# Optimization experiments

Measured on AMD Instinct MI355X. Metric: run time of the kernel, lower is better.

Reference implementation:

```python
import jax, jax.numpy as jnp
import numpy as np
from jax import lax

# --- static dims (match init_kwargs) ---
B = 16
Y, M, WIN = 10, 12, 48          # input_years, months_per_year, num_windows_per_month
T = Y * M * WIN                  # 5760 encoder timesteps
DENC = 256                       # encoder hidden size
U = 128                          # att_single_dense_units (bahdanau dim)
A1, A2 = 64, 32                  # att_single_dense_1st/2nd
K = 8                            # monthly/yearly num_kernels
KS, MPOOL, YPOOL = 3, 2, 2       # kernel_size, pool sizes (strides=1, VALID)
AMY = 64                         # att_mon_year_dense_1st
RNN = 256                        # RNN_num_units
FDEC = 64                        # dec_input features
NOUT = 64                        # n_output_features
# conv/pool output sizes (VALID conv, VALID pool stride 1)
H1, W1 = WIN - KS + 1 - MPOOL + 1, U - KS + 1 - MPOOL + 1      # 45, 125
H2, W2 = H1 - KS + 1 - MPOOL + 1, W1 - KS + 1 - MPOOL + 1      # 42, 122
FLATM = H2 * W2 * K                                            # 40992
HY, WY = M * H1 - KS + 1 - YPOOL + 1, W1 - KS + 1 - YPOOL + 1  # 537, 122
FLATY = HY * WY * K                                            # 524112


def conv_tanh(x, k, b):
    # Keras Conv2D(valid, activation='tanh'), NHWC/HWIO
    y = lax.conv_general_dilated(x, k, (1, 1), 'VALID',
                                 dimension_numbers=('NHWC', 'HWIO', 'NHWC'))
    return jnp.tanh(y + b)


def maxpool(x, p):
    # MaxPooling2D(pool_size=p, strides=1, valid)
    return lax.reduce_window(x, -jnp.inf, lax.max, (1, p, p, 1), (1, 1, 1, 1), 'VALID')


def setup_inputs() -> dict:
    key = jax.random.key(0)
    ks = jax.random.split(key, 24)
    r = lambda i, shape, s=0.02: jax.random.normal(ks[i], shape, jnp.float32) * s
    return {
        'dec_input': jax.random.normal(ks[0], (B, 1, FDEC), jnp.float32),
        'S_prev_dec': jax.random.normal(ks[1], (B, RNN), jnp.float32),
        'C_prev_dec': jax.random.normal(ks[2], (B, RNN), jnp.float32),
        'h_enc': jax.random.normal(ks[3], (B, T, DENC), jnp.float32),
        # attention_single params (all use_bias=False)
        'W_enc': r(4, (DENC, U)), 'W_dec': r(5, (RNN, U)),
        'W_att1': r(6, (U, A1)), 'W_att2': r(7, (A1, A2)), 'W_att3': r(8, (A2, 1)),
        # conv_pool layers
        'conv1_k': r(9, (KS, KS, 1, K)), 'conv1_b': jnp.zeros((K,), jnp.float32),
        'conv2_k': r(10, (KS, KS, K, K)), 'conv2_b': jnp.zeros((K,), jnp.float32),
        'convy_k': r(11, (KS, KS, K, K)), 'convy_b': jnp.zeros((K,), jnp.float32),
        # monthly / yearly attention denses (use_bias=True)
        'Wm1': r(12, (FLATM, AMY)), 'bm1': jnp.zeros((AMY,), jnp.float32),
        'Wm2': r(13, (AMY, 1)), 'bm2': jnp.zeros((1,), jnp.float32),
        'Wy1': r(14, (FLATY, AMY)), 'by1': jnp.zeros((AMY,), jnp.float32),
        'Wy2': r(15, (AMY, 1)), 'by2': jnp.zeros((1,), jnp.float32),
        # LSTM (input dim = DENC + FDEC); gate order i,f,g,o as in Keras
        'W_lstm': r(16, (DENC + FDEC, 4 * RNN)), 'U_lstm': r(17, (RNN, 4 * RNN)),
        'b_lstm': jnp.zeros((4 * RNN,), jnp.float32),
        # output dense
        'W_out': r(18, (RNN, NOUT)), 'b_out': jnp.zeros((NOUT,), jnp.float32),
    }


def reference(dec_input, S_prev_dec, C_prev_dec, h_enc,
              W_enc, W_dec, W_att1, W_att2, W_att3,
              conv1_k, conv1_b, conv2_k, conv2_b, convy_k, convy_b,
              Wm1, bm1, Wm2, bm2, Wy1, by1, Wy2, by2,
              W_lstm, U_lstm, b_lstm, W_out, b_out):
    # --- Bahdanau additive attention over all T encoder steps ---
    bah = h_enc @ W_enc + (S_prev_dec @ W_dec)[:, None, :]          # [B,T,U]
    e = jax.nn.relu(jax.nn.relu(jnp.tanh(bah @ W_att1) @ W_att2) @ W_att3)  # [B,T,1]
    aw = jax.nn.softmax(e, axis=1)[..., 0]                          # [B,T]
    # --- monthly conv-pool attention, batched over all Y*M month slices ---
    x = bah.reshape(B * Y * M, WIN, U, 1)
    c1 = maxpool(conv_tanh(x, conv1_k, conv1_b), MPOOL)             # [BYM,H1,W1,K]
    c2 = maxpool(conv_tanh(c1, conv2_k, conv2_b), MPOOL)            # [BYM,H2,W2,K]
    em = jax.nn.relu(jnp.tanh(c2.reshape(B * Y * M, FLATM) @ Wm1 + bm1) @ Wm2 + bm2)
    m_att = jax.nn.softmax(em.reshape(B, Y, M), axis=2)             # softmax over months
    # --- yearly conv-pool attention (months concatenated along height) ---
    yin = c1.reshape(B * Y, M * H1, W1, K)
    cy = maxpool(conv_tanh(yin, convy_k, convy_b), YPOOL)           # [BY,HY,WY,K]
    ey = jax.nn.relu(jnp.tanh(cy.reshape(B * Y, FLATY) @ Wy1 + by1) @ Wy2 + by2)
    y_att = jax.nn.softmax(ey.reshape(B, Y), axis=1)                # softmax over years
    # --- hierarchical combination of weights ---
    new_w = (aw.reshape(B, Y, M, WIN) * m_att[..., None]
             * y_att[:, :, None, None]).reshape(B, T)               # [B,T]
    ctx = jnp.einsum('bt,btd->bd', new_w, h_enc)                    # context [B,DENC]
    # --- single LSTM step on [context ; dec_input] ---
    xt = jnp.concatenate([ctx[:, None, :], dec_input], axis=-1)[:, 0, :]
    z = xt @ W_lstm + S_prev_dec @ U_lstm + b_lstm
    i, f, g, o = jnp.split(z, 4, axis=-1)
    c_new = jax.nn.sigmoid(f) * C_prev_dec + jax.nn.sigmoid(i) * jnp.tanh(g)
    h_new = jax.nn.sigmoid(o) * jnp.tanh(c_new)
    out = jax.nn.relu(h_new[:, None, :] @ W_out + b_out)            # [B,1,NOUT]
    return out, h_new, c_new, new_w
```

## Files before the change

kernel.cpp:

```cpp
#include <hip/hip_runtime.h>
#include <hip/hip_bf16.h>

#define DEV static __device__ __forceinline__

#define B_    16
#define Y_    10
#define M_    12
#define WIN_  48
#define T_    5760
#define DENC_ 256
#define U_    128
#define A1_   64
#define A2_   32
#define K_    8
#define RNN_  256
#define FDEC_ 64
#define NOUT_ 64

#define H1_   45
#define W1_   125
#define H2_   42
#define W2_   122
#define FLATM_ 40992
#define HY_   537
#define WY_   122
#define FLATY_ 524112
#define NSM_  1920
#define NSY_  160

typedef __attribute__((ext_vector_type(8))) short s16x8;
typedef __attribute__((ext_vector_type(4))) short s16x4;
typedef __attribute__((ext_vector_type(4))) float f32x4;

DEV float tanh_fast(float x){
  x = fminf(fmaxf(x, -15.0f), 15.0f);
  float e = __expf(2.0f*x);
  return (e - 1.0f) / (e + 1.0f);
}
DEV float tanh_nc(float x){
  float e = __expf(2.0f*x);
  return 1.0f - 2.0f/(e + 1.0f);
}
DEV float sigm(float x){ return 1.0f / (1.0f + __expf(-x)); }
DEV float wredsum(float v){
  #pragma unroll
  for (int off=32; off; off>>=1) v += __shfl_xor(v, off, 64);
  return v;
}
DEV short f2b(float f){
  __hip_bfloat16 h = __float2bfloat16(f);
  return *reinterpret_cast<short*>(&h);
}
DEV float b2f(short s){
  unsigned int x = ((unsigned int)(unsigned short)s) << 16;
  return __uint_as_float(x);
}
DEV unsigned int cvt_pk_bf16(float lo, float hi){
  unsigned int r;
  asm("v_cvt_pk_bf16_f32 %0, %1, %2" : "=v"(r) : "v"(lo), "v"(hi));
  return r;
}
DEV unsigned int swz_xor1u(unsigned int v){
  return (unsigned int)__builtin_amdgcn_ds_swizzle((int)v, 0x041F);
}
DEV unsigned int permb(unsigned int hi_src, unsigned int lo_src, unsigned int sel){
  return __builtin_amdgcn_perm(hi_src, lo_src, sel);
}

__global__ void k_cvt_bf16(const float* __restrict__ src, short* __restrict__ dst, long n4){
  long i = (long)blockIdx.x*256 + threadIdx.x;
  if (i < n4){
    f32x4 v = *(const f32x4*)(src + i*4);
    s16x4 o;
    #pragma unroll
    for (int q=0;q<4;q++) o[q] = f2b(v[q]);
    *(s16x4*)(dst + i*4) = o;
  }
}

__global__ void k_sdec(const float* __restrict__ S, const float* __restrict__ Wd,
                       float* __restrict__ sdec){
  int b = blockIdx.x, u = threadIdx.x;
  const float* s = S + b*DENC_;
  float acc = 0.f;
  #pragma unroll 4
  for (int d=0; d<DENC_; d++) acc += s[d]*Wd[d*U_+u];
  sdec[b*U_+u] = acc;
}

__global__ __launch_bounds__(256)
void k_bah_mfma(const float* __restrict__ h_enc, const short* __restrict__ Wenc_bf,
                const float* __restrict__ sdec, short* __restrict__ bah16){
  __shared__ short Wl[128*136];
  int tid = threadIdx.x;
  int m0 = blockIdx.x * 64;
  int lane = tid & 63, wid = tid >> 6;
  int pl = lane & 15, g = lane >> 4;
  long arow = m0 + wid*16 + pl;
  const float* ap = h_enc + arow*DENC_;
  f32x4 acc[8];
  #pragma unroll
  for (int i=0;i<8;i++) acc[i] = (f32x4){0.f,0.f,0.f,0.f};

  for (int kh=0; kh<2; kh++){
    for (int i=tid; i<16384; i+=256){
      int k = i >> 7, c = i & 127;
      Wl[c*136 + k] = Wenc_bf[(kh*128 + k)*U_ + c];
    }
    __syncthreads();
    #pragma unroll
    for (int kk=0; kk<4; kk++){
      f32x4 a0 = *(const f32x4*)(ap + kh*128 + kk*32 + g*8);
      f32x4 a1 = *(const f32x4*)(ap + kh*128 + kk*32 + g*8 + 4);
      s16x8 a;
      #pragma unroll
      for (int q=0;q<4;q++){ a[q] = f2b(a0[q]); a[4+q] = f2b(a1[q]); }
      #pragma unroll
      for (int nt=0; nt<8; nt++){
        s16x8 b = *(const s16x8*)(Wl + (nt*16+pl)*136 + kk*32 + g*8);
        acc[nt] = __builtin_amdgcn_mfma_f32_16x16x32_bf16(a, b, acc[nt], 0,0,0);
      }
    }
    __syncthreads();
  }
  int b = m0 / T_;
  #pragma unroll
  for (int nt=0; nt<8; nt++){
    float sd = sdec[b*U_ + nt*16 + pl];
    #pragma unroll
    for (int q=0; q<4; q++){
      long r = m0 + wid*16 + g*4 + q;
      bah16[r*U_ + nt*16 + pl] = f2b(acc[nt][q] + sd);
    }
  }
}

__global__ __launch_bounds__(256)
void k_att_mfma(const short* __restrict__ bah16, const float* __restrict__ W1,
                const float* __restrict__ W2, const float* __restrict__ W3f,
                float* __restrict__ e_out){
  __shared__ short W1l[64*136];
  __shared__ short W2l[32*72];
  __shared__ float hl[64][68];
  __shared__ float w3s[32];
  int tid = threadIdx.x;
  int lane = tid & 63, wid = tid >> 6;
  int pl = lane & 15, g = lane >> 4;
  long m0 = (long)blockIdx.x * 64;

  for (int i=tid; i<8192; i+=256){ int k=i>>6, c=i&63; W1l[c*136+k] = f2b(W1[k*64+c]); }
  for (int i=tid; i<2048; i+=256){ int k=i>>5, c=i&31; W2l[c*72+k]  = f2b(W2[k*32+c]); }
  if (tid < 32) w3s[tid] = W3f[tid];
  __syncthreads();

  const short* Ab = bah16 + (m0 + wid*16 + pl)*U_;
  f32x4 acc1[4];
  #pragma unroll
  for (int i=0;i<4;i++) acc1[i]=(f32x4){0.f,0.f,0.f,0.f};
  #pragma unroll
  for (int kk=0; kk<4; kk++){
    s16x8 a = *(const s16x8*)(Ab + kk*32 + g*8);
    #pragma unroll
    for (int nt=0; nt<4; nt++){
      s16x8 b = *(const s16x8*)(&W1l[(nt*16+pl)*136 + kk*32 + g*8]);
      acc1[nt] = __builtin_amdgcn_mfma_f32_16x16x32_bf16(a, b, acc1[nt], 0,0,0);
    }
  }
  #pragma unroll
  for (int nt=0; nt<4; nt++)
    #pragma unroll
    for (int q=0; q<4; q++)
      hl[wid*16 + g*4 + q][nt*16 + pl] = tanh_fast(acc1[nt][q]);
  __syncthreads();

  f32x4 acc2[2];
  #pragma unroll
  for (int i=0;i<2;i++) acc2[i]=(f32x4){0.f,0.f,0.f,0.f};
  #pragma unroll
  for (int kk=0; kk<2; kk++){
    f32x4 h0 = *(const f32x4*)(&hl[wid*16+pl][kk*32 + g*8]);
    f32x4 h1 = *(const f32x4*)(&hl[wid*16+pl][kk*32 + g*8 + 4]);
    s16x8 a;
    #pragma unroll
    for (int q=0;q<4;q++){ a[q]=f2b(h0[q]); a[4+q]=f2b(h1[q]); }
    #pragma unroll
    for (int nt=0; nt<2; nt++){
      s16x8 b = *(const s16x8*)(&W2l[(nt*16+pl)*72 + kk*32 + g*8]);
      acc2[nt] = __builtin_amdgcn_mfma_f32_16x16x32_bf16(a, b, acc2[nt], 0,0,0);
    }
  }
  #pragma unroll
  for (int q=0; q<4; q++){
    float v = fmaxf(acc2[0][q],0.f)*w3s[pl] + fmaxf(acc2[1][q],0.f)*w3s[16+pl];
    #pragma unroll
    for (int off=1; off<16; off<<=1) v += __shfl_xor(v, off, 64);
    if (pl == 0) e_out[m0 + wid*16 + g*4 + q] = fmaxf(v, 0.f);
  }
}

__global__ __launch_bounds__(256)
void k_softmax(const float* __restrict__ e, float* __restrict__ aw){
  int b = blockIdx.x, tid = threadIdx.x;
  __shared__ float red[4];
  const float* eb = e + (long)b*T_;
  float m = -1e30f;
  for (int t=tid; t<T_; t+=256) m = fmaxf(m, eb[t]);
  #pragma unroll
  for (int off=32; off; off>>=1) m = fmaxf(m, __shfl_xor(m, off, 64));
  if ((tid&63)==0) red[tid>>6] = m;
  __syncthreads();
  m = fmaxf(fmaxf(red[0],red[1]), fmaxf(red[2],red[3]));
  __syncthreads();
  float s = 0.f;
  for (int t=tid; t<T_; t+=256) s += __expf(eb[t]-m);
  s = wredsum(s);
  if ((tid&63)==0) red[tid>>6] = s;
  __syncthreads();
  s = red[0]+red[1]+red[2]+red[3];
  float inv = 1.0f/s;
  float* awb = aw + (long)b*T_;
  for (int t=tid; t<T_; t+=256) awb[t] = __expf(eb[t]-m)*inv;
}

__global__ __launch_bounds__(256)
void k_conv1s(const short* __restrict__ bah16, const float* __restrict__ k1,
              const float* __restrict__ b1, short* __restrict__ c1){
  int n = blockIdx.x >> 1, s = blockIdx.x & 1;
  int rp0 = s ? 23 : 0;
  int rp1 = s ? 44 : 22;
  int nin = rp1 + 4 - rp0;
  int tid = threadIdx.x;
  int lane = tid & 63, wid = tid >> 6;
  int c  = lane & 7;
  int wb = wid*8 + (lane >> 3);
  __shared__ float x[26][132];
  const short* xb = bah16 + (long)n*48*128 + rp0*128;
  for (int i=tid; i<nin*128; i+=256) x[i>>7][i&127] = b2f(xb[i]);
  for (int i=tid; i<26*4; i+=256)   x[i>>2][128+(i&3)] = 0.f;
  __syncthreads();

  float wk[9];
  #pragma unroll
  for (int p=0; p<9; p++) wk[p] = k1[p*8 + c];
  float bo = b1[c];
  bool odd = (c & 1);
  int qa = odd ? 2 : 0;
  bool va = (4*wb + qa)     <= 124;
  bool vb = (4*wb + qa + 1) <= 124;

  float rA[7], rB[7], rC[7];
  auto ldrow = [&](int rr, float* d){
    f32x4 a  = *(const f32x4*)(&x[rr][4*wb]);
    f32x4 b4 = *(const f32x4*)(&x[rr][4*wb+4]);
    d[0]=a[0]; d[1]=a[1]; d[2]=a[2]; d[3]=a[3]; d[4]=b4[0]; d[5]=b4[1]; d[6]=b4[2];
  };
  ldrow(0, rA); ldrow(1, rB);
  short* ob = c1 + (long)n*45*1000 + (long)rp0*1000;
  float vpc[4] = {0.f,0.f,0.f,0.f};
  int ncr = rp1 - rp0 + 2;

  for (int rr=0; rr<ncr; ++rr){
    ldrow(rr+2, rC);
    float cv[5];
    #pragma unroll
    for (int q=0; q<5; q++){
      cv[q] = bo + rA[q]*wk[0] + rA[q+1]*wk[1] + rA[q+2]*wk[2]
                 + rB[q]*wk[3] + rB[q+1]*wk[4] + rB[q+2]*wk[5]
                 + rC[q]*wk[6] + rC[q+1]*wk[7] + rC[q+2]*wk[8];
    }
    float wcv[4];
    #pragma unroll
    for (int q=0; q<4; q++) wcv[q] = fmaxf(cv[q], cv[q+1]);
    if (rr > 0){
      float t0 = tanh_nc(fmaxf(vpc[0], wcv[0]));
      float t1 = tanh_nc(fmaxf(vpc[1], wcv[1]));
      float t2 = tanh_nc(fmaxf(vpc[2], wcv[2]));
      float t3 = tanh_nc(fmaxf(vpc[3], wcv[3]));
      unsigned int A  = cvt_pk_bf16(t0, t1);
      unsigned int Bp = cvt_pk_bf16(t2, t3);
      unsigned int An = swz_xor1u(A);
      unsigned int Bn = swz_xor1u(Bp);
      unsigned int ph = odd ? Bp : An;
      unsigned int pw = odd ? Bn : A;
      unsigned int w0 = permb(ph, pw, 0x05040100u);
      unsigned int w1 = permb(ph, pw, 0x07060302u);
      long rbase = (long)(rr-1)*1000 + (c & ~1);
      if (va) *(unsigned int*)(ob + rbase + (4*wb+qa)*8)   = w0;
      if (vb) *(unsigned int*)(ob + rbase + (4*wb+qa+1)*8) = w1;
    }
    #pragma unroll
    for (int q=0; q<4; q++) vpc[q] = wcv[q];
    #pragma unroll
    for (int q=0; q<7; q++){ rA[q]=rB[q]; rB[q]=rC[q]; }
  }
}

#define LOADF(SL, OFF) { fa[SL] = *(const s16x8*)(gp + (OFF)); \
                         fb[SL] = *(const s16x8*)(gp + (OFF) + 128); }
#define CONVROW(SA,SB,SC, A0, A1) {                                          \
    A0 = (f32x4){0.f,0.f,0.f,0.f}; A1 = A0;                                  \
    A0 = __builtin_amdgcn_mfma_f32_16x16x32_bf16(fa[SA], bw[0], A0,0,0,0);   \
    A0 = __builtin_amdgcn_mfma_f32_16x16x32_bf16(fa[SB], bw[1], A0,0,0,0);   \
    A0 = __builtin_amdgcn_mfma_f32_16x16x32_bf16(fa[SC], bw[2], A0,0,0,0);   \
    A1 = __builtin_amdgcn_mfma_f32_16x16x32_bf16(fb[SA], bw[0], A1,0,0,0);   \
    A1 = __builtin_amdgcn_mfma_f32_16x16x32_bf16(fb[SB], bw[1], A1,0,0,0);   \
    A1 = __builtin_amdgcn_mfma_f32_16x16x32_bf16(fb[SC], bw[2], A1,0,0,0); }
#define PHASE(P) {                                                           \
    int ldr_ = base + (P) + 3; if (ldr_ > pmax_in) ldr_ = pmax_in;           \
    LOADF(((P)+3)&3, (long)(ldr_ - base)*1000);                              \
    f32x4 a0_, a1_;                                                          \
    CONVROW((P)&3, ((P)+1)&3, ((P)+2)&3, a0_, a1_);                          \
    epi(a0_, a1_, opg + (P)*976, base + (P));                                \
  }

__global__ __launch_bounds__(256)
void k_convf(const short* __restrict__ c1,
             const float* __restrict__ k2, const float* __restrict__ b2,
             const float* __restrict__ ky, const float* __restrict__ by,
             short* __restrict__ c2m, short* __restrict__ cy){
  int s  = blockIdx.x & 1;
  int nm = blockIdx.x >> 1;
  int n = nm / 12, m = nm % 12;
  int tid = threadIdx.x, lane = tid & 63, wid = tid >> 6;
  int pl = lane & 15, g = lane >> 4;
  bool isY = (pl >= 8);
  int ch = pl & 7;
  bool odd = (ch & 1);

  int rl_end = (m < 11) ? 45 : 42;
  int ps0 = s ? 23 : 0;
  int p1  = s ? rl_end : 23;
  int pmax_in = p1 + 2;

  const float* kern = isY ? ky : k2;
  s16x8 bw[3];
  #pragma unroll
  for (int dy=0; dy<3; dy++){
    #pragma unroll
    for (int i=0; i<8; i++){
      int k = g*8 + i;
      bw[dy][i] = (k < 24) ? f2b(kern[(dy*24 + k)*8 + ch]) : (short)0;
    }
  }
  float bo = isY ? by[ch] : b2[ch];

  int Tw = 31*wid;
  int qa = odd ? 2 : 0;
  int s0off = (Tw + g*4 + qa)*8 + (ch & ~1);
  bool v1a = (Tw + 16 + g*4 + qa)     <= 121;
  bool v1b = ((Tw + 16 + g*4 + qa + 1) <= 121) && !(odd && g == 3);
  int bpa16 = ((lane+16)&63)*4;
  int bpaPL = pl*4;

  const short* gp = c1 + ((long)n*540 + 45*m + ps0)*1000 + (size_t)((Tw + pl + g)*8);
  short* opg = isY ? (cy  + ((long)n*537 + (long)45*m + ps0 - 1)*976)
                   : (c2m + ((long)(n*12+m)*42 + ps0 - 1)*976);

  s16x8 fa[4], fb[4];
  LOADF(0, 0);
  LOADF(1, 1000);
  LOADF(2, 2000);

  float vp[8];
  #pragma unroll
  for (int i=0;i<8;i++) vp[i]=0.f;

  auto epi = [&](const f32x4& a0, const f32x4& a1, short* rowptr, int row){
    float n0 = __int_as_float(__builtin_amdgcn_ds_bpermute(bpa16, __float_as_int(a0[0])));
    float n1 = __int_as_float(__builtin_amdgcn_ds_bpermute(bpa16, __float_as_int(a1[0])));
    float nbv = __int_as_float(__builtin_amdgcn_ds_bpermute(bpaPL, __float_as_int(a1[0])));
    float nxt0 = (g < 3) ? n0 : nbv;
    float w[8];
    w[0]=fmaxf(a0[0],a0[1]); w[1]=fmaxf(a0[1],a0[2]);
    w[2]=fmaxf(a0[2],a0[3]); w[3]=fmaxf(a0[3],nxt0);
    w[4]=fmaxf(a1[0],a1[1]); w[5]=fmaxf(a1[1],a1[2]);
    w[6]=fmaxf(a1[2],a1[3]); w[7]=fmaxf(a1[3],n1);
    bool en = (row > ps0) && (isY || row <= 42);
    if (en){
      float t0 = tanh_nc(fmaxf(vp[0], w[0]) + bo);
      float t1 = tanh_nc(fmaxf(vp[1], w[1]) + bo);
      float t2 = tanh_nc(fmaxf(vp[2], w[2]) + bo);
      float t3 = tanh_nc(fmaxf(vp[3], w[3]) + bo);
      float t4 = tanh_nc(fmaxf(vp[4], w[4]) + bo);
      float t5 = tanh_nc(fmaxf(vp[5], w[5]) + bo);
      float t6 = tanh_nc(fmaxf(vp[6], w[6]) + bo);
      float t7 = tanh_nc(fmaxf(vp[7], w[7]) + bo);
      unsigned int A  = cvt_pk_bf16(t0, t1);
      unsigned int Bp = cvt_pk_bf16(t2, t3);
      unsigned int An = swz_xor1u(A);
      unsigned int Bn = swz_xor1u(Bp);
      unsigned int ph = odd ? Bp : An;
      unsigned int pw = odd ? Bn : A;
      unsigned int d0 = permb(ph, pw, 0x05040100u);
      unsigned int d1 = permb(ph, pw, 0x07060302u);
      unsigned int C  = cvt_pk_bf16(t4, t5);
      unsigned int Dp = cvt_pk_bf16(t6, t7);
      unsigned int Cn = swz_xor1u(C);
      unsigned int Dn = swz_xor1u(Dp);
      unsigned int qh = odd ? Dp : Cn;
      unsigned int qw = odd ? Dn : C;
      unsigned int d2 = permb(qh, qw, 0x05040100u);
      unsigned int d3 = permb(qh, qw, 0x07060302u);
      *(unsigned int*)(rowptr + s0off)       = d0;
      *(unsigned int*)(rowptr + s0off + 8)   = d1;
      if (v1a) *(unsigned int*)(rowptr + s0off + 128) = d2;
      if (v1b) *(unsigned int*)(rowptr + s0off + 136) = d3;
    }
    #pragma unroll
    for (int i=0;i<8;i++) vp[i] = w[i];
  };

  int base = ps0;
  for (; base + 3 <= p1; base += 4){
    PHASE(0)
    PHASE(1)
    PHASE(2)
    PHASE(3)
    gp += 4000; opg += 4*976;
  }
  int rem = p1 - base + 1;
  if (rem > 0){ PHASE(0) }
  if (rem > 1){ PHASE(1) }
  if (rem > 2){ PHASE(2) }
}
#undef PHASE
#undef CONVROW
#undef LOADF

__global__ void k_init64(float* __restrict__ C, const float* __restrict__ bias, int n){
  int i = blockIdx.x*256 + threadIdx.x;
  if (i < n) C[i] = bias[i & 63];
}

__global__ __launch_bounds__(256)
void k_gemm64m(const __hip_bfloat16* __restrict__ A, const float* __restrict__ W,
               float* __restrict__ C, int Mrows, long Kdim, int mtiles, int spc){
  __shared__ short Ws_t[2][64*72];
  int mt = blockIdx.x % mtiles;
  int kc = blockIdx.x / mtiles;
  long nsteps = (Kdim + 63) >> 6;
  long s0 = (long)kc * spc;
  if (s0 >= nsteps) return;
  long s1 = min(nsteps, s0 + (long)spc);
  int m0 = mt * 64;
  int tid = threadIdx.x;
  int lane = tid & 63, wid = tid >> 6;
  int pl = lane & 15, g = lane >> 4;
  long arow = m0 + wid*16 + pl;
  if (arow >= Mrows) arow = 0;
  const short* Ab = (const short*)A + arow*Kdim;
  int wc = tid & 63, wk0 = (tid >> 6)*2;
  f32x4 acc[4];
  #pragma unroll
  for (int i=0;i<4;i++) acc[i]=(f32x4){0.f,0.f,0.f,0.f};

  float wr[16];
  auto loadW = [&](long s, float* w){
    long kb = s << 6;
    #pragma unroll
    for (int j=0;j<8;j++){
      long kg = kb + wk0 + j*8;
      w[2*j]   = (kg   < Kdim) ? W[kg*64 + wc]     : 0.f;
      w[2*j+1] = (kg+1 < Kdim) ? W[(kg+1)*64 + wc] : 0.f;
    }
  };
  auto writeW = [&](int buf, const float* w){
    #pragma unroll
    for (int j=0;j<8;j++){
      unsigned int p = cvt_pk_bf16(w[2*j], w[2*j+1]);
      *(unsigned int*)(&Ws_t[buf][wc*72 + wk0 + j*8]) = p;
    }
  };
  s16x8 aA[2], aN[2];
  auto loadA = [&](long s, s16x8* a){
    long kb = s << 6;
    #pragma unroll
    for (int kk=0;kk<2;kk++){
      long ko = kb + kk*32 + g*8;
      a[kk] = (ko < Kdim) ? *(const s16x8*)(Ab + ko) : (s16x8){0,0,0,0,0,0,0,0};
    }
  };

  loadW(s0, wr);
  loadA(s0, aA);
  writeW(0, wr);
  __syncthreads();
  int cur = 0;
  for (long s = s0; s < s1; ++s){
    bool more = (s+1 < s1);
    float wrn[16];
    if (more){ loadW(s+1, wrn); loadA(s+1, aN); }
    #pragma unroll
    for (int kk=0; kk<2; kk++){
      #pragma unroll
      for (int nt=0; nt<4; nt++){
        s16x8 b = *(const s16x8*)(&Ws_t[cur][(nt*16+pl)*72 + kk*32 + g*8]);
        acc[nt] = __builtin_amdgcn_mfma_f32_16x16x32_bf16(aA[kk], b, acc[nt], 0,0,0);
      }
    }
    if (more){
      __syncthreads();
      writeW(cur^1, wrn);
      __syncthreads();
      aA[0] = aN[0]; aA[1] = aN[1];
      cur ^= 1;
    }
  }
  #pragma unroll
  for (int nt=0; nt<4; nt++){
    #pragma unroll
    for (int q=0; q<4; q++){
      int r = m0 + wid*16 + g*4 + q;
      if (r < Mrows) atomicAdd(&C[(long)r*64 + nt*16 + pl], acc[nt][q]);
    }
  }
}

__global__ void k_month_head(const float* __restrict__ em_pre, const float* __restrict__ Wm2,
                             const float* __restrict__ bm2, float* __restrict__ m_att){
  int g = blockIdx.x;
  int tid = threadIdx.x;
  __shared__ float em[M_];
  float w2 = Wm2[tid];
  for (int m=0; m<M_; m++){
    float v = tanh_fast(em_pre[(g*M_+m)*64 + tid]) * w2;
    v = wredsum(v);
    if (tid==0) em[m] = fmaxf(v + bm2[0], 0.f);
  }
  __syncthreads();
  if (tid==0){
    float mx = -1e30f;
    for (int m=0;m<M_;m++) mx = fmaxf(mx, em[m]);
    float s=0.f; float ex[M_];
    for (int m=0;m<M_;m++){ ex[m]=__expf(em[m]-mx); s+=ex[m]; }
    float inv = 1.0f/s;
    for (int m=0;m<M_;m++) m_att[g*M_+m] = ex[m]*inv;
  }
}

__global__ void k_year_head(const float* __restrict__ ey_pre, const float* __restrict__ Wy2,
                            const float* __restrict__ by2, float* __restrict__ y_att){
  int b = blockIdx.x;
  int tid = threadIdx.x;
  __shared__ float ey[Y_];
  float w2 = Wy2[tid];
  for (int y=0; y<Y_; y++){
    float v = tanh_fast(ey_pre[(b*Y_+y)*64 + tid]) * w2;
    v = wredsum(v);
    if (tid==0) ey[y] = fmaxf(v + by2[0], 0.f);
  }
  __syncthreads();
  if (tid==0){
    float mx = -1e30f;
    for (int y=0;y<Y_;y++) mx = fmaxf(mx, ey[y]);
    float s=0.f; float ex[Y_];
    for (int y=0;y<Y_;y++){ ex[y]=__expf(ey[y]-mx); s+=ex[y]; }
    float inv = 1.0f/s;
    for (int y=0;y<Y_;y++) y_att[b*Y_+y] = ex[y]*inv;
  }
}

__global__ void k_new_w(const float* __restrict__ aw, const float* __restrict__ m_att,
                        const float* __restrict__ y_att, float* __restrict__ nw){
  int idx = blockIdx.x*256 + threadIdx.x;
  if (idx < B_*T_){
    int b = idx / T_, t = idx % T_;
    int y = t / (M_*WIN_), m = (t % (M_*WIN_)) / WIN_;
    nw[idx] = aw[idx] * m_att[(b*Y_+y)*M_+m] * y_att[b*Y_+y];
  }
}

__global__ void k_zero(float* __restrict__ p, int n){
  int i = blockIdx.x*256 + threadIdx.x; if (i<n) p[i]=0.f;
}

__global__ __launch_bounds__(256)
void k_ctx(const float* __restrict__ nw, const float* __restrict__ h_enc,
           float* __restrict__ ctx){
  int b = blockIdx.x >> 6, ch = blockIdx.x & 63;
  int d = threadIdx.x;
  float acc = 0.f;
  int t0 = ch*(T_/64), t1 = t0 + (T_/64);
  for (int t=t0; t<t1; t++)
    acc += nw[b*T_+t] * h_enc[((long)b*T_+t)*DENC_ + d];
  atomicAdd(&ctx[b*DENC_+d], acc);
}

__global__ void k_lstm_z(const float* __restrict__ ctx, const float* __restrict__ dec,
                         const float* __restrict__ S, const float* __restrict__ Wl,
                         const float* __restrict__ Ul, const float* __restrict__ bl,
                         float* __restrict__ z){
  int b = blockIdx.x >> 2;
  int j = (blockIdx.x & 3)*256 + threadIdx.x;
  float acc = bl[j];
  const float* cb = ctx + b*DENC_;
  const float* db = dec + b*FDEC_;
  const float* sb = S + b*RNN_;
  #pragma unroll 4
  for (int d=0; d<DENC_; d++) acc += cb[d]*Wl[d*1024 + j];
  #pragma unroll 4
  for (int d=0; d<FDEC_; d++) acc += db[d]*Wl[(DENC_+d)*1024 + j];
  #pragma unroll 4
  for (int d=0; d<RNN_; d++) acc += sb[d]*Ul[d*1024 + j];
  z[b*1024 + j] = acc;
}

__global__ void k_gates(const float* __restrict__ z, const float* __restrict__ Cprev,
                        float* __restrict__ h_out, float* __restrict__ c_out){
  int b = blockIdx.x, j = threadIdx.x;
  const float* zb = z + b*1024;
  float iv = sigm(zb[j]);
  float fv = sigm(zb[256+j]);
  float gv = tanh_fast(zb[512+j]);
  float ov = sigm(zb[768+j]);
  float c = fv*Cprev[b*RNN_+j] + iv*gv;
  float h = ov*tanh_fast(c);
  h_out[b*RNN_+j] = h;
  c_out[b*RNN_+j] = c;
}

__global__ void k_out(const float* __restrict__ h, const float* __restrict__ Wo,
                      const float* __restrict__ bo, float* __restrict__ out){
  int b = blockIdx.x, q = threadIdx.x;
  float acc = bo[q];
  #pragma unroll 4
  for (int j=0; j<RNN_; j++) acc += h[b*RNN_+j]*Wo[j*64+q];
  out[b*64+q] = fmaxf(acc, 0.f);
}

extern "C" void kernel_launch(void* const* d_in, const int* in_sizes, int n_in,
                              void* d_out, int out_size, void* d_ws, size_t ws_size,
                              hipStream_t stream){
  const float* dec_input = (const float*)d_in[0];
  const float* S_prev = (const float*)d_in[1];
  const float* C_prev = (const float*)d_in[2];
  const float* h_enc  = (const float*)d_in[3];
  const float* W_enc  = (const float*)d_in[4];
  const float* W_dec  = (const float*)d_in[5];
  const float* W_att1 = (const float*)d_in[6];
  const float* W_att2 = (const float*)d_in[7];
  const float* W_att3 = (const float*)d_in[8];
  const float* conv1_k= (const float*)d_in[9];
  const float* conv1_b= (const float*)d_in[10];
  const float* conv2_k= (const float*)d_in[11];
  const float* conv2_b= (const float*)d_in[12];
  const float* convy_k= (const float*)d_in[13];
  const float* convy_b= (const float*)d_in[14];
  const float* Wm1    = (const float*)d_in[15];
  const float* bm1    = (const float*)d_in[16];
  const float* Wm2    = (const float*)d_in[17];
  const float* bm2    = (const float*)d_in[18];
  const float* Wy1    = (const float*)d_in[19];
  const float* by1    = (const float*)d_in[20];
  const float* Wy2    = (const float*)d_in[21];
  const float* by2    = (const float*)d_in[22];
  const float* W_lstm = (const float*)d_in[23];
  const float* U_lstm = (const float*)d_in[24];
  const float* b_lstm = (const float*)d_in[25];
  const float* W_out  = (const float*)d_in[26];
  const float* b_out  = (const float*)d_in[27];

  char* ws = (char*)d_ws;
  size_t off = 0;
  auto alloc = [&](size_t bytes)->char*{
    char* p = ws + off; off += (bytes + 255) & ~(size_t)255; return p;
  };
  short* bah16          = (short*)alloc((size_t)B_*T_*U_*2);
  short* c1             = (short*)alloc((size_t)NSM_*H1_*W1_*K_*2);
  short* c2m            = (short*)alloc((size_t)NSM_*H2_*W2_*K_*2);
  short* cy             = (short*)alloc((size_t)NSY_*HY_*WY_*K_*2);
  float* e              = (float*)alloc((size_t)B_*T_*4);
  float* aw             = (float*)alloc((size_t)B_*T_*4);
  float* sdec           = (float*)alloc(B_*U_*4);
  float* em_pre         = (float*)alloc(NSM_*64*4);
  float* ey_pre         = (float*)alloc(NSY_*64*4);
  float* m_att          = (float*)alloc(NSM_*4);
  float* y_att          = (float*)alloc(NSY_*4);
  float* ctx            = (float*)alloc(B_*DENC_*4);
  float* zbuf           = (float*)alloc(B_*1024*4);
  short* Wenc_bf        = (short*)alloc(DENC_*U_*2);

  float* out   = (float*)d_out;
  float* h_new = out + 1024;
  float* c_new = h_new + 4096;
  float* nw    = c_new + 4096;

  k_cvt_bf16<<<(DENC_*U_/4 + 255)/256, 256, 0, stream>>>(W_enc, Wenc_bf, DENC_*U_/4);
  k_sdec<<<B_, U_, 0, stream>>>(S_prev, W_dec, sdec);
  k_bah_mfma<<<(B_*T_)/64, 256, 0, stream>>>(h_enc, Wenc_bf, sdec, bah16);
  k_att_mfma<<<(B_*T_)/64, 256, 0, stream>>>(bah16, W_att1, W_att2, W_att3, e);
  k_softmax<<<B_, 256, 0, stream>>>(e, aw);
  k_conv1s<<<NSM_*2, 256, 0, stream>>>(bah16, conv1_k, conv1_b, c1);
  k_convf<<<NSY_*12*2, 256, 0, stream>>>(c1, conv2_k, conv2_b, convy_k, convy_b, c2m, cy);
  k_init64<<<(NSM_*64+255)/256, 256, 0, stream>>>(em_pre, bm1, NSM_*64);
  k_gemm64m<<<81*30, 256, 0, stream>>>((const __hip_bfloat16*)c2m, Wm1, em_pre, NSM_, (long)FLATM_, 30, 8);
  k_month_head<<<NSY_, 64, 0, stream>>>(em_pre, Wm2, bm2, m_att);
  k_init64<<<(NSY_*64+255)/256, 256, 0, stream>>>(ey_pre, by1, NSY_*64);
  k_gemm64m<<<512*3, 256, 0, stream>>>((const __hip_bfloat16*)cy, Wy1, ey_pre, NSY_, (long)FLATY_, 3, 16);
  k_year_head<<<B_, 64, 0, stream>>>(ey_pre, Wy2, by2, y_att);
  k_new_w<<<(B_*T_+255)/256, 256, 0, stream>>>(aw, m_att, y_att, nw);
  k_zero<<<(B_*DENC_+255)/256, 256, 0, stream>>>(ctx, B_*DENC_);
  k_ctx<<<B_*64, 256, 0, stream>>>(nw, h_enc, ctx);
  k_lstm_z<<<B_*4, 256, 0, stream>>>(ctx, dec_input, S_prev, W_lstm, U_lstm, b_lstm, zbuf);
  k_gates<<<B_, 256, 0, stream>>>(zbuf, C_prev, h_new, c_new);
  k_out<<<B_, 64, 0, stream>>>(h_new, W_out, b_out, out);
}
```

Before: 654.5 us.

## Move first monthly conv onto bf16 MFMA with separate edge-column kernel

Replaces the scalar FP32 LDS-based 3x3 conv+maxpool+tanh for the monthly first layer with an MFMA formulation. Input rows are loaded directly from global memory into a rotating 4-slot register pipeline, and the 2x2 pool is done via ds_bpermute plus a running previous-row max. The last output column that the MFMA tiling does not cover is computed by a new small scalar kernel. This adds a kernel launch and rounds the conv weights to bf16, and it relies on exact column coverage being handled correctly.

```diff
diff --git a/kernel.cpp b/kernel.cpp
--- a/kernel.cpp
+++ b/kernel.cpp
@@ -222,76 +222,129 @@
   for (int t=tid; t<T_; t+=256) awb[t] = __expf(eb[t]-m)*inv;
 }
 
+#define C1LOAD(SL, LR) { \
+    fa[SL] = *(const s16x8*)(xb + (long)((LR)+g)*128 + Tw + pl); \
+    fb[SL] = *(const s16x8*)(xb + (long)((LR)+g)*128 + Tw + 16 + pl); }
+#define C1PHASE(P) { \
+    int ldr_ = base + (P) + 3; if (ldr_ > p1) ldr_ = p1; \
+    C1LOAD(((P)+3)&3, ldr_); \
+    f32x4 A0 = (f32x4){0.f,0.f,0.f,0.f}, A1 = A0; \
+    A0 = __builtin_amdgcn_mfma_f32_16x16x32_bf16(fa[(P)&3], bw, A0, 0,0,0); \
+    A1 = __builtin_amdgcn_mfma_f32_16x16x32_bf16(fb[(P)&3], bw, A1, 0,0,0); \
+    epi(A0, A1, opg + (P)*1000, base + (P)); }
+
 __global__ __launch_bounds__(256)
-void k_conv1s(const short* __restrict__ bah16, const float* __restrict__ k1,
+void k_conv1m(const short* __restrict__ bah16, const float* __restrict__ k1,
               const float* __restrict__ b1, short* __restrict__ c1){
-  int n = blockIdx.x >> 1, s = blockIdx.x & 1;
-  int rp0 = s ? 23 : 0;
-  int rp1 = s ? 44 : 22;
-  int nin = rp1 + 4 - rp0;
-  int tid = threadIdx.x;
-  int lane = tid & 63, wid = tid >> 6;
-  int c  = lane & 7;
-  int wb = wid*8 + (lane >> 3);
-  __shared__ float x[26][132];
-  const short* xb = bah16 + (long)n*48*128 + rp0*128;
-  for (int i=tid; i<nin*128; i+=256) x[i>>7][i&127] = b2f(xb[i]);
-  for (int i=tid; i<26*4; i+=256)   x[i>>2][128+(i&3)] = 0.f;
-  __syncthreads();
-
-  float wk[9];
-  #pragma unroll
-  for (int p=0; p<9; p++) wk[p] = k1[p*8 + c];
-  float bo = b1[c];
-  bool odd = (c & 1);
+  int s = blockIdx.x & 1;
+  int n = blockIdx.x >> 1;
+  int tid = threadIdx.x, lane = tid & 63, wid = tid >> 6;
+  int pl = lane & 15, g = lane >> 4;
+  int ch = pl & 7;
+  bool hi = (pl >= 8);
+  bool odd = (ch & 1);
+
+  int ps0 = s ? 23 : 0;
+  int p1  = s ? 45 : 23;
+
+  s16x8 bw;
+  #pragma unroll
+  for (int i=0; i<8; i++)
+    bw[i] = (g < 3 && i < 3) ? f2b(k1[(g*3 + i)*8 + ch]) : (short)0;
+  float bo = b1[ch];
+
+  int Tw = 31*wid;
   int qa = odd ? 2 : 0;
-  bool va = (4*wb + qa)     <= 124;
-  bool vb = (4*wb + qa + 1) <= 124;
-
-  float rA[7], rB[7], rC[7];
-  auto ldrow = [&](int rr, float* d){
-    f32x4 a  = *(const f32x4*)(&x[rr][4*wb]);
-    f32x4 b4 = *(const f32x4*)(&x[rr][4*wb+4]);
-    d[0]=a[0]; d[1]=a[1]; d[2]=a[2]; d[3]=a[3]; d[4]=b4[0]; d[5]=b4[1]; d[6]=b4[2];
-  };
-  ldrow(0, rA); ldrow(1, rB);
-  short* ob = c1 + (long)n*45*1000 + (long)rp0*1000;
-  float vpc[4] = {0.f,0.f,0.f,0.f};
-  int ncr = rp1 - rp0 + 2;
-
-  for (int rr=0; rr<ncr; ++rr){
-    ldrow(rr+2, rC);
-    float cv[5];
-    #pragma unroll
-    for (int q=0; q<5; q++){
-      cv[q] = bo + rA[q]*wk[0] + rA[q+1]*wk[1] + rA[q+2]*wk[2]
-                 + rB[q]*wk[3] + rB[q+1]*wk[4] + rB[q+2]*wk[5]
-                 + rC[q]*wk[6] + rC[q+1]*wk[7] + rC[q+2]*wk[8];
-    }
-    float wcv[4];
-    #pragma unroll
-    for (int q=0; q<4; q++) wcv[q] = fmaxf(cv[q], cv[q+1]);
-    if (rr > 0){
-      float t0 = tanh_nc(fmaxf(vpc[0], wcv[0]));
-      float t1 = tanh_nc(fmaxf(vpc[1], wcv[1]));
-      float t2 = tanh_nc(fmaxf(vpc[2], wcv[2]));
-      float t3 = tanh_nc(fmaxf(vpc[3], wcv[3]));
+  int pixb = Tw + (hi ? 16 : 0) + 4*g + qa;
+  int sbase = pixb*8 + (ch & ~1);
+  bool vd1 = !(hi && odd && g == 3);
+  int bpa = ((lane + 16) & 63) * 4;
+
+  const short* xb = bah16 + (long)n*48*128;
+  short* opg = c1 + (long)n*45*1000 + (long)(ps0 - 1)*1000;
+
+  s16x8 fa[4], fb[4];
+  C1LOAD(0, ps0);
+  C1LOAD(1, ps0+1);
+  C1LOAD(2, ps0+2);
+
+  float vp[4] = {0.f,0.f,0.f,0.f};
+
+  auto epi = [&](const f32x4& A0, const f32x4& A1, short* rowptr, int row){
+    float a0q = hi ? A1[0] : A0[0];
+    float a1q = hi ? A1[1] : A0[1];
+    float a2q = hi ? A1[2] : A0[2];
+    float a3q = hi ? A1[3] : A0[3];
+    float nb = __int_as_float(__builtin_amdgcn_ds_bpermute(bpa, __float_as_int(a0q)));
+    float nxt3 = (g == 3) ? A1[0] : nb;
+    float w0 = fmaxf(a0q, a1q);
+    float w1 = fmaxf(a1q, a2q);
+    float w2 = fmaxf(a2q, a3q);
+    float w3 = fmaxf(a3q, nxt3);
+    if (row > ps0){
+      float t0 = tanh_nc(fmaxf(vp[0], w0) + bo);
+      float t1 = tanh_nc(fmaxf(vp[1], w1) + bo);
+      float t2 = tanh_nc(fmaxf(vp[2], w2) + bo);
+      float t3 = tanh_nc(fmaxf(vp[3], w3) + bo);
       unsigned int A  = cvt_pk_bf16(t0, t1);
       unsigned int Bp = cvt_pk_bf16(t2, t3);
       unsigned int An = swz_xor1u(A);
       unsigned int Bn = swz_xor1u(Bp);
       unsigned int ph = odd ? Bp : An;
       unsigned int pw = odd ? Bn : A;
-      unsigned int w0 = permb(ph, pw, 0x05040100u);
-      unsigned int w1 = permb(ph, pw, 0x07060302u);
-      long rbase = (long)(rr-1)*1000 + (c & ~1);
-      if (va) *(unsigned int*)(ob + rbase + (4*wb+qa)*8)   = w0;
-      if (vb) *(unsigned int*)(ob + rbase + (4*wb+qa+1)*8) = w1;
-    }
-    #pragma unroll
-    for (int q=0; q<4; q++) vpc[q] = wcv[q];
-    #pragma unroll
-    for (int q=0; q<7; q++){ rA[q]=rB[q]; rB[q]=rC[q]; }
+      unsigned int d0 = permb(ph, pw, 0x05040100u);
+      unsigned int d1 = permb(ph, pw, 0x07060302u);
+      *(unsigned int*)(rowptr + sbase) = d0;
+      if (vd1) *(unsigned int*)(rowptr + sbase + 8) = d1;
+    }
+    vp[0]=w0; vp[1]=w1; vp[2]=w2; vp[3]=w3;
+  };
+
+  int base = ps0;
+  for (; base + 3 <= p1; base += 4){
+    C1PHASE(0)
+    C1PHASE(1)
+    C1PHASE(2)
+    C1PHASE(3)
+    opg += 4*1000;
+  }
+  int rem = p1 - base + 1;
+  if (rem > 0){ C1PHASE(0) }
+  if (rem > 1){ C1PHASE(1) }
+  if (rem > 2){ C1PHASE(2) }
+}
+#undef C1PHASE
+#undef C1LOAD
+
+__global__ void k_c1edge(const short* __restrict__ bah16, const float* __restrict__ k1,
+                         const float* __restrict__ b1, short* __restrict__ c1){
+  int idx = blockIdx.x*256 + threadIdx.x;
+  if (idx >= NSM_*45) return;
+  int n = idx / 45, r = idx % 45;
+  const short* xb = bah16 + (long)n*48*128;
+  float x[4][4];
+  #pragma unroll
+  for (int i=0;i<4;i++)
+    #pragma unroll
+    for (int j=0;j<4;j++) x[i][j] = b2f(xb[(long)(r+i)*128 + 124 + j]);
+  short* ob = c1 + (long)n*45*1000 + (long)r*1000 + 124*8;
+  #pragma unroll
+  for (int c=0;c<8;c++){
+    float best = -1e30f;
+    #pragma unroll
+    for (int pr=0; pr<2; pr++){
+      #pragma unroll
+      for (int px=0; px<2; px++){
+        float v = 0.f;
+        #pragma unroll
+        for (int dy=0;dy<3;dy++)
+          #pragma unroll
+          for (int dx=0;dx<3;dx++)
+            v += x[pr+dy][px+dx] * k1[(dy*3+dx)*8 + c];
+        best = fmaxf(best, v);
+      }
+    }
+    ob[c] = f2b(tanh_nc(best + b1[c]));
   }
 }
 
@@ -690,7 +743,8 @@
   k_bah_mfma<<<(B_*T_)/64, 256, 0, stream>>>(h_enc, Wenc_bf, sdec, bah16);
   k_att_mfma<<<(B_*T_)/64, 256, 0, stream>>>(bah16, W_att1, W_att2, W_att3, e);
   k_softmax<<<B_, 256, 0, stream>>>(e, aw);
-  k_conv1s<<<NSM_*2, 256, 0, stream>>>(bah16, conv1_k, conv1_b, c1);
+  k_conv1m<<<NSM_*2, 256, 0, stream>>>(bah16, conv1_k, conv1_b, c1);
+  k_c1edge<<<(NSM_*45 + 255)/256, 256, 0, stream>>>(bah16, conv1_k, conv1_b, c1);
   k_convf<<<NSY_*12*2, 256, 0, stream>>>(c1, conv2_k, conv2_b, convy_k, convy_b, c2m, cy);
   k_init64<<<(NSM_*64+255)/256, 256, 0, stream>>>(em_pre, bm1, NSM_*64);
   k_gemm64m<<<81*30, 256, 0, stream>>>((const __hip_bfloat16*)c2m, Wm1, em_pre, NSM_, (long)FLATM_, 30, 8);
```

Measured after the change: 700.1 us. 1.07x slower.
